# Optimization experiments

Hardware: AMD Instinct MI355X
Metric: run time of the kernel (lower is better)

The kernel has to match this reference:

```python
import jax, jax.numpy as jnp
import numpy as np

B, C_IN, H, W = 4, 16, 64, 64
OUT_C, K, STRIDE = 32, 3, 1
NUM_DEG = 6   # numerator coeffs for x^0..x^5 (order[0]+1)
DEN_DEG = 4


def setup_inputs() -> dict:
    key = jax.random.key(0)
    k1, k2, k3 = jax.random.split(key, 3)
    x = jax.random.normal(k1, (B, C_IN, H, W), dtype=jnp.float32)
    nums = 0.1 * jax.random.normal(k2, (OUT_C * C_IN * K * K, NUM_DEG), dtype=jnp.float32)
    denoms = 0.1 * jax.random.normal(k3, (OUT_C * C_IN * K * K, DEN_DEG), dtype=jnp.float32)
    return {"input": x, "nums": nums, "denoms": denoms}


def _ka_conv(x, nums, denoms):
    pad = (K - 1) // 2
    xp = jnp.pad(x, ((0, 0), (0, 0), (pad, pad), (pad, pad)))
    Ho = (x.shape[2] + 2 * pad - K) // STRIDE + 1
    Wo = (x.shape[3] + 2 * pad - K) // STRIDE + 1
    # patches [B, C, K*K, Ho, Wo] ordered (c, ki, kj) to match nums row layout
    patches = jnp.stack(
        [xp[:, :, i:i + STRIDE * Ho:STRIDE, j:j + STRIDE * Wo:STRIDE]
         for i in range(K) for j in range(K)], axis=2)
    M = C_IN * K * K
    patches = patches.reshape(x.shape[0], M, Ho, Wo)
    # powers x^0..x^5 built by cumulative products (grad-safe at x=0)
    pows = [jnp.ones_like(patches)]
    for _ in range(NUM_DEG - 1):
        pows.append(pows[-1] * patches)
    pw = jnp.stack(pows, axis=-1)  # [B, M, Ho, Wo, NUM_DEG]
    a = nums.reshape(OUT_C, M, NUM_DEG)
    b = denoms.reshape(OUT_C, M, DEN_DEG)
    # per-weight rational: P/Q for every (out_channel, weight, position)
    num = jnp.einsum('bmhwp,omp->bomhw', pw, a)
    den = 1.0 + jnp.abs(jnp.einsum('bmhwq,omq->bomhw', pw[..., 1:1 + DEN_DEG], b))
    return jnp.sum(num / den, axis=2)  # [B, OUT_C, Ho, Wo]


def reference(input, nums, denoms):
    return _ka_conv(input, nums, denoms)
```

## Files before the change

kernel.cpp:

```cpp
#include <hip/hip_runtime.h>


constexpr int Bn = 4, Cin = 16, Hh = 64, Ww = 64, Oc = 32, Mtot = 144;

__global__ __launch_bounds__(256, 2)
void ka_conv_kernel(const float* __restrict__ x,
                    const float* __restrict__ nums,
                    const float* __restrict__ denoms,
                    float* __restrict__ out) {
  const int tid = threadIdx.x;
  const int w  = tid & 63;
  const int rg = tid >> 6;
  int blk = blockIdx.x;
  const int ht = blk & 3;  blk >>= 2;
  const int o  = blk & 31; blk >>= 5;
  const int b  = blk;
  const int h0 = ht * 16 + rg * 4;

  const float* __restrict__ an = nums   + (size_t)o * Mtot * 6;
  const float* __restrict__ bd = denoms + (size_t)o * Mtot * 4;

  float acc0 = 0.f, acc1 = 0.f, acc2 = 0.f, acc3 = 0.f;

  #pragma unroll 2
  for (int c = 0; c < Cin; ++c) {
    const float* __restrict__ xc = x + (size_t)(b * Cin + c) * (Hh * Ww);
    float X[6][3];
    #pragma unroll
    for (int i = 0; i < 6; ++i) {
      const int  hr  = h0 - 1 + i;
      const int  hc  = min(max(hr, 0), Hh - 1);
      const bool hin = (unsigned)hr < (unsigned)Hh;
      #pragma unroll
      for (int j = 0; j < 3; ++j) {
        const int  wc  = w - 1 + j;
        const int  wcc = min(max(wc, 0), Ww - 1);
        const bool win = (unsigned)wc < (unsigned)Ww;
        const float v  = xc[hc * Ww + wcc];
        X[i][j] = (hin && win) ? v : 0.f;
      }
    }
    #pragma unroll
    for (int ki = 0; ki < 3; ++ki) {
      #pragma unroll
      for (int kj = 0; kj < 3; ++kj) {
        const int m = c * 9 + ki * 3 + kj;
        const float* a  = an + m * 6;
        const float* bq = bd + m * 4;
        const float a0 = a[0], a1 = a[1], a2 = a[2], a3 = a[3], a4 = a[4], a5 = a[5];
        const float b1 = bq[0], b2 = bq[1], b3 = bq[2], b4 = bq[3];
        #pragma unroll
        for (int p = 0; p < 4; ++p) {
          const float v = X[p + ki][kj];
          float num = fmaf(fmaf(fmaf(fmaf(fmaf(a5, v, a4), v, a3), v, a2), v, a1), v, a0);
          float dp  = fmaf(fmaf(fmaf(b4, v, b3), v, b2), v, b1) * v;
          float den = 1.0f + fabsf(dp);
          float r   = __builtin_amdgcn_rcpf(den);
          float t   = num * r;
          if      (p == 0) acc0 += t;
          else if (p == 1) acc1 += t;
          else if (p == 2) acc2 += t;
          else             acc3 += t;
        }
      }
    }
  }

  float* op = out + ((size_t)(b * Oc + o) * Hh + h0) * Ww + w;
  op[0 * Ww] = acc0;
  op[1 * Ww] = acc1;
  op[2 * Ww] = acc2;
  op[3 * Ww] = acc3;
}

extern "C" void kernel_launch(void* const* d_in, const int* in_sizes, int n_in,
                              void* d_out, int out_size, void* d_ws, size_t ws_size,
                              hipStream_t stream) {
  const float* x      = (const float*)d_in[0];
  const float* nums   = (const float*)d_in[1];
  const float* denoms = (const float*)d_in[2];
  float* out          = (float*)d_out;
  dim3 grid(Bn * Oc * 4);
  ka_conv_kernel<<<grid, 256, 0, stream>>>(x, nums, denoms, out);
}
```

Baseline: 34.94 us.

## Stage coefficients in LDS, halve rows per thread, double-buffer channel patch loads

Each block first copies its output channel's numerator and denominator coefficients into shared memory, so they are read from LDS instead of through scalar or global loads. Each thread now computes 2 output rows instead of 4, which doubles the grid to 1024 blocks and raises the launch-bounds occupancy hint to 4. Input patches are double-buffered across channels so the next channel's loads are issued before the current channel is computed. The cost is more redundant halo loads per output (4 rows loaded for 2 outputs instead of 6 for 4) plus an extra block-wide sync.

```diff
diff --git a/kernel.cpp b/kernel.cpp
--- a/kernel.cpp
+++ b/kernel.cpp
@@ -3,31 +3,40 @@
 
 constexpr int Bn = 4, Cin = 16, Hh = 64, Ww = 64, Oc = 32, Mtot = 144;
 
-__global__ __launch_bounds__(256, 2)
+__global__ __launch_bounds__(256, 4)
 void ka_conv_kernel(const float* __restrict__ x,
                     const float* __restrict__ nums,
                     const float* __restrict__ denoms,
                     float* __restrict__ out) {
+  __shared__ float sA[Mtot * 6];
+  __shared__ float sB[Mtot * 4];
+
   const int tid = threadIdx.x;
+  int blk = blockIdx.x;
+  const int ht = blk & 7;  blk >>= 3;
+  const int o  = blk & 31; blk >>= 5;
+  const int b  = blk;
+
+  {
+    const float* __restrict__ an = nums   + (size_t)o * Mtot * 6;
+    const float* __restrict__ bd = denoms + (size_t)o * Mtot * 4;
+    for (int i = tid; i < Mtot * 6; i += 256) sA[i] = an[i];
+    for (int i = tid; i < Mtot * 4; i += 256) sB[i] = bd[i];
+  }
+  __syncthreads();
+
   const int w  = tid & 63;
   const int rg = tid >> 6;
-  int blk = blockIdx.x;
-  const int ht = blk & 3;  blk >>= 2;
-  const int o  = blk & 31; blk >>= 5;
-  const int b  = blk;
-  const int h0 = ht * 16 + rg * 4;
+  const int h0 = ht * 8 + rg * 2;
 
-  const float* __restrict__ an = nums   + (size_t)o * Mtot * 6;
-  const float* __restrict__ bd = denoms + (size_t)o * Mtot * 4;
+  float acc0 = 0.f, acc1 = 0.f;
 
-  float acc0 = 0.f, acc1 = 0.f, acc2 = 0.f, acc3 = 0.f;
+  const float* __restrict__ xb = x + (size_t)b * Cin * Hh * Ww;
 
-  #pragma unroll 2
-  for (int c = 0; c < Cin; ++c) {
-    const float* __restrict__ xc = x + (size_t)(b * Cin + c) * (Hh * Ww);
-    float X[6][3];
+  auto load_patch = [&](int c, float X[4][3]) {
+    const float* __restrict__ xc = xb + (size_t)c * (Hh * Ww);
     #pragma unroll
-    for (int i = 0; i < 6; ++i) {
+    for (int i = 0; i < 4; ++i) {
       const int  hr  = h0 - 1 + i;
       const int  hc  = min(max(hr, 0), Hh - 1);
       const bool hin = (unsigned)hr < (unsigned)Hh;
@@ -40,37 +49,45 @@
         X[i][j] = (hin && win) ? v : 0.f;
       }
     }
+  };
+
+  auto compute = [&](int c, const float X[4][3]) {
+    const int mbase = c * 9;
     #pragma unroll
     for (int ki = 0; ki < 3; ++ki) {
       #pragma unroll
       for (int kj = 0; kj < 3; ++kj) {
-        const int m = c * 9 + ki * 3 + kj;
-        const float* a  = an + m * 6;
-        const float* bq = bd + m * 4;
-        const float a0 = a[0], a1 = a[1], a2 = a[2], a3 = a[3], a4 = a[4], a5 = a[5];
-        const float b1 = bq[0], b2 = bq[1], b3 = bq[2], b4 = bq[3];
+        const int m = mbase + ki * 3 + kj;
+        const float a0 = sA[m * 6 + 0], a1 = sA[m * 6 + 1], a2 = sA[m * 6 + 2];
+        const float a3 = sA[m * 6 + 3], a4 = sA[m * 6 + 4], a5 = sA[m * 6 + 5];
+        const float b1 = sB[m * 4 + 0], b2 = sB[m * 4 + 1];
+        const float b3 = sB[m * 4 + 2], b4 = sB[m * 4 + 3];
         #pragma unroll
-        for (int p = 0; p < 4; ++p) {
+        for (int p = 0; p < 2; ++p) {
           const float v = X[p + ki][kj];
           float num = fmaf(fmaf(fmaf(fmaf(fmaf(a5, v, a4), v, a3), v, a2), v, a1), v, a0);
           float dp  = fmaf(fmaf(fmaf(b4, v, b3), v, b2), v, b1) * v;
           float den = 1.0f + fabsf(dp);
           float r   = __builtin_amdgcn_rcpf(den);
-          float t   = num * r;
-          if      (p == 0) acc0 += t;
-          else if (p == 1) acc1 += t;
-          else if (p == 2) acc2 += t;
-          else             acc3 += t;
+          if (p == 0) acc0 = fmaf(num, r, acc0);
+          else        acc1 = fmaf(num, r, acc1);
         }
       }
     }
+  };
+
+  float X0[4][3], X1[4][3];
+  load_patch(0, X0);
+  for (int c = 0; c < Cin; c += 2) {
+    load_patch(c + 1, X1);
+    compute(c, X0);
+    if (c + 2 < Cin) load_patch(c + 2, X0);
+    compute(c + 1, X1);
   }
 
   float* op = out + ((size_t)(b * Oc + o) * Hh + h0) * Ww + w;
-  op[0 * Ww] = acc0;
-  op[1 * Ww] = acc1;
-  op[2 * Ww] = acc2;
-  op[3 * Ww] = acc3;
+  op[0]  = acc0;
+  op[Ww] = acc1;
 }
 
 extern "C" void kernel_launch(void* const* d_in, const int* in_sizes, int n_in,
@@ -80,6 +97,6 @@
   const float* nums   = (const float*)d_in[1];
   const float* denoms = (const float*)d_in[2];
   float* out          = (float*)d_out;
-  dim3 grid(Bn * Oc * 4);
+  dim3 grid(Bn * Oc * 8);
   ka_conv_kernel<<<grid, 256, 0, stream>>>(x, nums, denoms, out);
 }
```

Result: slower. 75.71 us (+116.7%).
